# Kernel optimization log

Measured on AMD Instinct MI355X. Metric: run time of the kernel, lower is better.

Reference implementation:

```python
import jax, jax.numpy as jnp
import numpy as np

WINDOW = 7
NUM_HEADS = 12

def _relative_position_index(ws: int) -> np.ndarray:
    coords = np.stack(np.meshgrid(np.arange(ws), np.arange(ws), indexing='ij'))  # (2, ws, ws)
    flat = coords.reshape(2, -1)  # (2, N)
    rel = flat[:, :, None] - flat[:, None, :]  # (2, N, N)
    rel = rel.transpose(1, 2, 0).copy()
    rel[:, :, 0] += ws - 1
    rel[:, :, 1] += ws - 1
    rel[:, :, 0] *= 2 * ws - 1
    return rel.sum(-1)  # (N, N) int

REL_IDX = jnp.asarray(_relative_position_index(WINDOW))  # (49, 49)

def setup_inputs() -> dict:
    key = jax.random.key(0)
    ks = jax.random.split(key, 7)
    B_, N, C = 2048, 49, 384
    nW = 64
    return {
        'x': jax.random.normal(ks[0], (B_, N, C), jnp.float32),
        'mask': jax.random.normal(ks[1], (nW, N, N), jnp.float32),
        'qkv_w': jax.random.normal(ks[2], (3 * C, C), jnp.float32) * 0.02,
        'qkv_b': jax.random.normal(ks[3], (3 * C,), jnp.float32) * 0.02,
        'proj_w': jax.random.normal(ks[4], (C, C), jnp.float32) * 0.02,
        'proj_b': jax.random.normal(ks[5], (C,), jnp.float32) * 0.02,
        'rel_bias_table': jax.random.normal(ks[6], ((2 * WINDOW - 1) ** 2, NUM_HEADS), jnp.float32) * 0.02,
    }

def reference(x, mask, qkv_w, qkv_b, proj_w, proj_b, rel_bias_table):
    B_, N, C = x.shape
    H = NUM_HEADS
    D = C // H
    scale = D ** -0.5
    # fused qkv projection: (B_, N, 3C) -> (3, B_, H, N, D)
    qkv = (x @ qkv_w.T + qkv_b).reshape(B_, N, 3, H, D).transpose(2, 0, 3, 1, 4)
    q, k, v = qkv[0], qkv[1], qkv[2]
    attn = jnp.einsum('bhnd,bhmd->bhnm', q, k) * scale  # (B_, H, N, N)
    # relative position bias gather: (N, N, H) -> (H, N, N)
    bias = rel_bias_table[REL_IDX].transpose(2, 0, 1)
    attn = attn + bias[None]
    nW = mask.shape[0]
    B = B_ // nW
    attn = attn.reshape(B, nW, H, N, N) + mask[None, :, None]
    attn = attn.reshape(B_, H, N, N)
    attn = jax.nn.softmax(attn, axis=-1)
    out = jnp.einsum('bhnm,bhmd->bnhd', attn, v).reshape(B_, N, C)
    return out @ proj_w.T + proj_b
```

## Files before the change

kernel.cpp:

```cpp
#include <hip/hip_runtime.h>
#include <hip/hip_bf16.h>
#include <stdint.h>
#include <stddef.h>

typedef __attribute__((ext_vector_type(8))) short short8;
typedef __attribute__((ext_vector_type(4))) float floatx4;

#define GLDS16(gptr, lptr)                                                         \
  __builtin_amdgcn_global_load_lds(                                                \
      (const __attribute__((address_space(1))) void*)(gptr),                       \
      (__attribute__((address_space(3))) void*)(lptr), 16, 0, 0)

#define MTOT  100352
#define KDIM  384
#define NQKV  1152
#define NPROJ 384

static __device__ __forceinline__ unsigned short bfu(float f) {
    __hip_bfloat16 h = __float2bfloat16(f);
    return *(unsigned short*)&h;
}

__global__ void cvt_kernel(const float* __restrict__ in,
                           __hip_bfloat16* __restrict__ out, int n4) {
    int i = blockIdx.x * blockDim.x + threadIdx.x;
    if (i >= n4) return;
    float4 v = ((const float4*)in)[i];
    __hip_bfloat16* o = out + (size_t)i * 4;
    o[0] = __float2bfloat16(v.x);
    o[1] = __float2bfloat16(v.y);
    o[2] = __float2bfloat16(v.z);
    o[3] = __float2bfloat16(v.w);
}

__global__ void build_bias_kernel(const float* __restrict__ tbl,
                                  const float* __restrict__ mask,
                                  float* __restrict__ comb) {
    int tid = blockIdx.x * 256 + threadIdx.x;
    if (tid >= 12 * 64 * 49 * 52) return;
    int hw = tid / 2548;
    int nm = tid - hw * 2548;
    int row = nm / 52;
    int col = nm - row * 52;
    int h = hw >> 6;
    int w2 = hw & 63;
    float v = -1e30f;
    if (col < 49) {
        int i1 = row / 7, j1 = row - i1 * 7;
        int i2 = col / 7, j2 = col - i2 * 7;
        int ridx = (i1 - i2 + 6) * 13 + (j1 - j2 + 6);
        v = tbl[ridx * 12 + h] + mask[(size_t)w2 * 2401 + row * 49 + col];
    }
    comb[tid] = v;
}

template <int EPI>
__global__ __launch_bounds__(256, 4) void gemm_bt_kernel(
    const __hip_bfloat16* __restrict__ A, const __hip_bfloat16* __restrict__ B,
    const float* __restrict__ bias, float* __restrict__ Cout,
    __hip_bfloat16* __restrict__ qbuf, __hip_bfloat16* __restrict__ kbuf,
    __hip_bfloat16* __restrict__ vbuf, int N, int NBN, int vt_mode) {
    __shared__ __hip_bfloat16 sA[128 * 64];
    __shared__ __hip_bfloat16 sB[128 * 64];
    const int t = threadIdx.x;
    const int per_chunk = 16 * NBN;
    const int chunk = blockIdx.x / per_chunk;
    const int rr = blockIdx.x - chunk * per_chunk;
    const int bn = rr >> 4;
    const int bm = chunk * 16 + (rr & 15);

    const int lane = t & 63;
    const int w = t >> 6;
    const int wm = w & 1, wn = w >> 1;
    const int quad = lane >> 4, l15 = lane & 15;
    const int srow = t >> 3;
    const int scg = t & 7;
    const int sg = scg ^ (srow & 7);
    const int rsw = l15 & 7;

    const __hip_bfloat16* Ab = A + (size_t)bm * 128 * KDIM;
    const __hip_bfloat16* Bb = B + (size_t)bn * 128 * KDIM;

    const floatx4 fzero = {0.f, 0.f, 0.f, 0.f};
    floatx4 acc[4][4];
#pragma unroll
    for (int i = 0; i < 4; ++i)
#pragma unroll
        for (int j = 0; j < 4; ++j) acc[i][j] = fzero;

    for (int kk = 0; kk < KDIM; kk += 64) {
#pragma unroll
        for (int i = 0; i < 4; ++i) {
            const int r0 = srow + i * 32;
            GLDS16(Ab + (size_t)r0 * KDIM + kk + sg * 8, &sA[r0 * 64 + scg * 8]);
            GLDS16(Bb + (size_t)r0 * KDIM + kk + sg * 8, &sB[r0 * 64 + scg * 8]);
        }
        __syncthreads();
#pragma unroll
        for (int kk2 = 0; kk2 < 2; ++kk2) {
            short8 af[4], bf[4];
#pragma unroll
            for (int i = 0; i < 4; ++i)
                af[i] = *(const short8*)&sA[(wm * 64 + i * 16 + l15) * 64 +
                                            ((kk2 * 4 + quad) ^ rsw) * 8];
#pragma unroll
            for (int j = 0; j < 4; ++j)
                bf[j] = *(const short8*)&sB[(wn * 64 + j * 16 + l15) * 64 +
                                            ((kk2 * 4 + quad) ^ rsw) * 8];
#pragma unroll
            for (int i = 0; i < 4; ++i)
#pragma unroll
                for (int j = 0; j < 4; ++j)
                    acc[i][j] = __builtin_amdgcn_mfma_f32_16x16x32_bf16(
                        af[i], bf[j], acc[i][j], 0, 0, 0);
        }
        __syncthreads();
    }

    int colv[4];
    float bv4[4];
#pragma unroll
    for (int j = 0; j < 4; ++j) {
        colv[j] = bn * 128 + wn * 64 + j * 16 + l15;
        bv4[j] = bias[colv[j]];
    }

    if (EPI == 0) {
        const float scale = 0.17677669529663687f;
        int partv[4], hv4[4], dv4[4];
#pragma unroll
        for (int j = 0; j < 4; ++j) {
            partv[j] = colv[j] >= 768 ? 2 : (colv[j] >= 384 ? 1 : 0);
            int within = colv[j] - partv[j] * 384;
            hv4[j] = within >> 5;
            dv4[j] = within & 31;
        }
#pragma unroll
        for (int i = 0; i < 4; ++i) {
#pragma unroll
            for (int r = 0; r < 4; ++r) {
                const int row = bm * 128 + wm * 64 + i * 16 + quad * 4 + r;
                const int b = row / 49;
                const int nn = row - b * 49;
#pragma unroll
                for (int j = 0; j < 4; ++j) {
                    const float val = acc[i][j][r] + bv4[j];
                    const size_t bh = (size_t)b * 12 + hv4[j];
                    if (partv[j] == 0)
                        qbuf[(bh * 49 + nn) * 32 + dv4[j]] =
                            __float2bfloat16(val * scale);
                    else if (partv[j] == 1)
                        kbuf[(bh * 49 + nn) * 32 + dv4[j]] = __float2bfloat16(val);
                    else {
                        if (vt_mode)
                            vbuf[(bh * 32 + dv4[j]) * 56 + nn] = __float2bfloat16(val);
                        else
                            vbuf[(bh * 49 + nn) * 32 + dv4[j]] = __float2bfloat16(val);
                    }
                }
            }
        }
    } else {
#pragma unroll
        for (int i = 0; i < 4; ++i) {
#pragma unroll
            for (int r = 0; r < 4; ++r) {
                const int row = bm * 128 + wm * 64 + i * 16 + quad * 4 + r;
#pragma unroll
                for (int j = 0; j < 4; ++j)
                    Cout[(size_t)row * N + colv[j]] = acc[i][j][r] + bv4[j];
            }
        }
    }
}

template <int VT>
__global__ __launch_bounds__(64) void attn_kernel(
    const __hip_bfloat16* __restrict__ qbuf,
    const __hip_bfloat16* __restrict__ kbuf,
    const __hip_bfloat16* __restrict__ vslab,
    const float* __restrict__ comb,
    __hip_bfloat16* __restrict__ attn_out) {
    __shared__ unsigned short sP[64 * 72];
    const int id = blockIdx.x;
    const int h = id >> 11;
    const int rem = id & 2047;
    const int w = rem >> 5;
    const int b = rem & 31;
    const int b_ = b * 64 + w;
    const int lane = threadIdx.x;
    const int quad = lane >> 4, l15 = lane & 15;
    const size_t bh = (size_t)b_ * 12 + h;
    const short* qb = (const short*)qbuf + bh * 1568;
    const short* kb = (const short*)kbuf + bh * 1568;
    const short* vb = (const short*)vslab + bh * (VT ? 1792 : 1568);

    const floatx4 fzero = {0.f, 0.f, 0.f, 0.f};

    short8 bQ[4], aK[4];
#pragma unroll
    for (int im = 0; im < 4; ++im) {
        int m = im * 16 + l15;
        m = m > 48 ? 48 : m;
        bQ[im] = *(const short8*)(qb + m * 32 + quad * 8);
    }
#pragma unroll
    for (int jn = 0; jn < 4; ++jn) {
        int n = jn * 16 + l15;
        n = n > 48 ? 48 : n;
        aK[jn] = *(const short8*)(kb + n * 32 + quad * 8);
    }

    floatx4 ST[4][4];
#pragma unroll
    for (int im = 0; im < 4; ++im)
#pragma unroll
        for (int jn = 0; jn < 4; ++jn)
            ST[im][jn] = __builtin_amdgcn_mfma_f32_16x16x32_bf16(aK[jn], bQ[im],
                                                                 fzero, 0, 0, 0);

    const float* cb = comb + (size_t)(h * 64 + w) * 2548;
#pragma unroll
    for (int im = 0; im < 4; ++im) {
        const int m = im * 16 + l15;
        const int mrow = m > 48 ? 48 : m;
        const float* rp = cb + mrow * 52;
        float v[16];
#pragma unroll
        for (int jn = 0; jn < 3; ++jn) {
            float4 c4 = *(const float4*)(rp + jn * 16 + quad * 4);
            v[jn * 4 + 0] = ST[im][jn][0] + c4.x;
            v[jn * 4 + 1] = ST[im][jn][1] + c4.y;
            v[jn * 4 + 2] = ST[im][jn][2] + c4.z;
            v[jn * 4 + 3] = ST[im][jn][3] + c4.w;
        }
        {
            const float s48 = rp[48];
            v[12] = (quad == 0) ? (ST[im][3][0] + s48) : -1e30f;
            v[13] = -1e30f;
            v[14] = -1e30f;
            v[15] = -1e30f;
        }
        float mx = v[0];
#pragma unroll
        for (int q = 1; q < 16; ++q) mx = fmaxf(mx, v[q]);
        mx = fmaxf(mx, __shfl_xor(mx, 16));
        mx = fmaxf(mx, __shfl_xor(mx, 32));
        float sum = 0.f;
#pragma unroll
        for (int q = 0; q < 16; ++q) {
            v[q] = __expf(v[q] - mx);
            sum += v[q];
        }
        sum += __shfl_xor(sum, 16);
        sum += __shfl_xor(sum, 32);
        const float inv = 1.0f / sum;
#pragma unroll
        for (int jn = 0; jn < 4; ++jn) {
            uint2 pk;
            pk.x = (unsigned int)bfu(v[jn * 4 + 0] * inv) |
                   ((unsigned int)bfu(v[jn * 4 + 1] * inv) << 16);
            pk.y = (unsigned int)bfu(v[jn * 4 + 2] * inv) |
                   ((unsigned int)bfu(v[jn * 4 + 3] * inv) << 16);
            *(uint2*)&sP[m * 72 + jn * 16 + quad * 4] = pk;
        }
    }
    __syncthreads();

    short8 aP[4][2];
#pragma unroll
    for (int im = 0; im < 4; ++im)
#pragma unroll
        for (int kk = 0; kk < 2; ++kk)
            aP[im][kk] =
                *(const short8*)&sP[(im * 16 + l15) * 72 + kk * 32 + quad * 8];

    short8 bV[2][2];
    if (VT) {
#pragma unroll
        for (int jd = 0; jd < 2; ++jd)
#pragma unroll
            for (int kk = 0; kk < 2; ++kk) {
                int n0 = kk * 32 + quad * 8;
                n0 = n0 > 48 ? 48 : n0;
                bV[jd][kk] = *(const short8*)(vb + (jd * 16 + l15) * 56 + n0);
            }
    } else {
#pragma unroll
        for (int jd = 0; jd < 2; ++jd)
#pragma unroll
            for (int kk = 0; kk < 2; ++kk) {
                short8 tmp;
#pragma unroll
                for (int jj = 0; jj < 8; ++jj) {
                    int k = kk * 32 + quad * 8 + jj;
                    k = k > 48 ? 48 : k;
                    tmp[jj] = vb[k * 32 + jd * 16 + l15];
                }
                bV[jd][kk] = tmp;
            }
    }

    floatx4 O[4][2];
#pragma unroll
    for (int im = 0; im < 4; ++im)
#pragma unroll
        for (int jd = 0; jd < 2; ++jd) {
            floatx4 o = __builtin_amdgcn_mfma_f32_16x16x32_bf16(aP[im][0], bV[jd][0],
                                                                fzero, 0, 0, 0);
            o = __builtin_amdgcn_mfma_f32_16x16x32_bf16(aP[im][1], bV[jd][1], o, 0,
                                                        0, 0);
            O[im][jd] = o;
        }

#pragma unroll
    for (int im = 0; im < 4; ++im) {
#pragma unroll
        for (int r = 0; r < 4; ++r) {
            const int m = im * 16 + quad * 4 + r;
            if (m < 49) {
#pragma unroll
                for (int jd = 0; jd < 2; ++jd)
                    attn_out[((size_t)b_ * 49 + m) * 384 + h * 32 + jd * 16 + l15] =
                        __float2bfloat16(O[im][jd][r]);
            }
        }
    }
}

extern "C" void kernel_launch(void* const* d_in, const int* in_sizes, int n_in,
                              void* d_out, int out_size, void* d_ws,
                              size_t ws_size, hipStream_t stream) {
    (void)in_sizes; (void)n_in; (void)out_size;
    const float* x      = (const float*)d_in[0];
    const float* mask   = (const float*)d_in[1];
    const float* qkv_w  = (const float*)d_in[2];
    const float* qkv_b  = (const float*)d_in[3];
    const float* proj_w = (const float*)d_in[4];
    const float* proj_b = (const float*)d_in[5];
    const float* tbl    = (const float*)d_in[6];
    float* out = (float*)d_out;
    char* ws = (char*)d_ws;

    __hip_bfloat16* x_bf  = (__hip_bfloat16*)(ws);
    __hip_bfloat16* wq_bf = (__hip_bfloat16*)(ws + 77070336);
    float*          comb  = (float*)(ws + 77070336);
    __hip_bfloat16* wp_bf = (__hip_bfloat16*)(ws + 84897792);
    __hip_bfloat16* q_buf = (__hip_bfloat16*)(ws + 85192704);
    __hip_bfloat16* k_buf = (__hip_bfloat16*)(ws + 162263040);
    __hip_bfloat16* v_slab = (__hip_bfloat16*)(ws + 239333376);
    __hip_bfloat16* attn_out = x_bf;

    const int vt = (ws_size >= (size_t)327413760) ? 1 : 0;

    cvt_kernel<<<(MTOT * KDIM / 4 + 255) / 256, 256, 0, stream>>>(x, x_bf,
                                                                  MTOT * KDIM / 4);
    cvt_kernel<<<(NQKV * KDIM / 4 + 255) / 256, 256, 0, stream>>>(
        qkv_w, wq_bf, NQKV * KDIM / 4);
    cvt_kernel<<<(NPROJ * KDIM / 4 + 255) / 256, 256, 0, stream>>>(
        proj_w, wp_bf, NPROJ * KDIM / 4);
    gemm_bt_kernel<0><<<784 * 9, 256, 0, stream>>>(x_bf, wq_bf, qkv_b, nullptr,
                                                   q_buf, k_buf, v_slab, NQKV, 9,
                                                   vt);
    build_bias_kernel<<<(12 * 64 * 49 * 52 + 255) / 256, 256, 0, stream>>>(
        tbl, mask, comb);
    if (vt)
        attn_kernel<1><<<2048 * 12, 64, 0, stream>>>(q_buf, k_buf, v_slab, comb,
                                                     attn_out);
    else
        attn_kernel<0><<<2048 * 12, 64, 0, stream>>>(q_buf, k_buf, v_slab, comb,
                                                     attn_out);
    gemm_bt_kernel<1><<<784 * 3, 256, 0, stream>>>(attn_out, wp_bf, proj_b, out,
                                                   nullptr, nullptr, nullptr,
                                                   NPROJ, 3, 0);
}
```

Measured before the change: 612.5 us.

## Store QKV as row-major bf16 with vectorized epilogues and stage V via LDS

The QKV GEMM now writes a plain row-major bf16 [M,1152] buffer. Swapping the MFMA operands lets each lane hold four consecutive columns, so the epilogue packs them into 8-byte stores instead of scattered 2-byte writes into per-head Q/K/V layouts. The projection GEMM epilogue likewise uses float4 stores. The attention kernel reads Q/K/V with strided row loads, stages V through shared memory to transpose it, and writes its output as packed 8-byte stores. This trades strided reads in attention, which touch many rows at a 2304-byte stride, for coalesced GEMM epilogue writes and drops the transposed-V workspace path.

Result: faster. 557.8 us (-8.9%).

```diff
diff --git a/kernel.cpp b/kernel.cpp
--- a/kernel.cpp
+++ b/kernel.cpp
@@ -16,9 +16,9 @@
 #define NQKV  1152
 #define NPROJ 384
 
-static __device__ __forceinline__ unsigned short bfu(float f) {
+static __device__ __forceinline__ unsigned int bfu(float f) {
     __hip_bfloat16 h = __float2bfloat16(f);
-    return *(unsigned short*)&h;
+    return (unsigned int)*(unsigned short*)&h;
 }
 
 __global__ void cvt_kernel(const float* __restrict__ in,
@@ -58,8 +58,7 @@
 __global__ __launch_bounds__(256, 4) void gemm_bt_kernel(
     const __hip_bfloat16* __restrict__ A, const __hip_bfloat16* __restrict__ B,
     const float* __restrict__ bias, float* __restrict__ Cout,
-    __hip_bfloat16* __restrict__ qbuf, __hip_bfloat16* __restrict__ kbuf,
-    __hip_bfloat16* __restrict__ vbuf, int N, int NBN, int vt_mode) {
+    __hip_bfloat16* __restrict__ Cbf, int N, int NBN) {
     __shared__ __hip_bfloat16 sA[128 * 64];
     __shared__ __hip_bfloat16 sB[128 * 64];
     const int t = threadIdx.x;
@@ -112,76 +111,54 @@
 #pragma unroll
                 for (int j = 0; j < 4; ++j)
                     acc[i][j] = __builtin_amdgcn_mfma_f32_16x16x32_bf16(
-                        af[i], bf[j], acc[i][j], 0, 0, 0);
+                        bf[j], af[i], acc[i][j], 0, 0, 0);
         }
         __syncthreads();
-    }
-
-    int colv[4];
-    float bv4[4];
-#pragma unroll
-    for (int j = 0; j < 4; ++j) {
-        colv[j] = bn * 128 + wn * 64 + j * 16 + l15;
-        bv4[j] = bias[colv[j]];
     }
 
     if (EPI == 0) {
         const float scale = 0.17677669529663687f;
-        int partv[4], hv4[4], dv4[4];
-#pragma unroll
-        for (int j = 0; j < 4; ++j) {
-            partv[j] = colv[j] >= 768 ? 2 : (colv[j] >= 384 ? 1 : 0);
-            int within = colv[j] - partv[j] * 384;
-            hv4[j] = within >> 5;
-            dv4[j] = within & 31;
-        }
 #pragma unroll
         for (int i = 0; i < 4; ++i) {
-#pragma unroll
-            for (int r = 0; r < 4; ++r) {
-                const int row = bm * 128 + wm * 64 + i * 16 + quad * 4 + r;
-                const int b = row / 49;
-                const int nn = row - b * 49;
-#pragma unroll
-                for (int j = 0; j < 4; ++j) {
-                    const float val = acc[i][j][r] + bv4[j];
-                    const size_t bh = (size_t)b * 12 + hv4[j];
-                    if (partv[j] == 0)
-                        qbuf[(bh * 49 + nn) * 32 + dv4[j]] =
-                            __float2bfloat16(val * scale);
-                    else if (partv[j] == 1)
-                        kbuf[(bh * 49 + nn) * 32 + dv4[j]] = __float2bfloat16(val);
-                    else {
-                        if (vt_mode)
-                            vbuf[(bh * 32 + dv4[j]) * 56 + nn] = __float2bfloat16(val);
-                        else
-                            vbuf[(bh * 49 + nn) * 32 + dv4[j]] = __float2bfloat16(val);
-                    }
-                }
+            const int m = bm * 128 + wm * 64 + i * 16 + l15;
+#pragma unroll
+            for (int j = 0; j < 4; ++j) {
+                const int f0 = bn * 128 + wn * 64 + j * 16 + quad * 4;
+                const float4 bv = *(const float4*)&bias[f0];
+                const float sc = (f0 < 384) ? scale : 1.0f;
+                uint2 pk;
+                pk.x = bfu((acc[i][j][0] + bv.x) * sc) |
+                       (bfu((acc[i][j][1] + bv.y) * sc) << 16);
+                pk.y = bfu((acc[i][j][2] + bv.z) * sc) |
+                       (bfu((acc[i][j][3] + bv.w) * sc) << 16);
+                *(uint2*)&Cbf[(size_t)m * NQKV + f0] = pk;
             }
         }
     } else {
 #pragma unroll
         for (int i = 0; i < 4; ++i) {
-#pragma unroll
-            for (int r = 0; r < 4; ++r) {
-                const int row = bm * 128 + wm * 64 + i * 16 + quad * 4 + r;
-#pragma unroll
-                for (int j = 0; j < 4; ++j)
-                    Cout[(size_t)row * N + colv[j]] = acc[i][j][r] + bv4[j];
+            const int m = bm * 128 + wm * 64 + i * 16 + l15;
+#pragma unroll
+            for (int j = 0; j < 4; ++j) {
+                const int f0 = bn * 128 + wn * 64 + j * 16 + quad * 4;
+                const float4 bv = *(const float4*)&bias[f0];
+                float4 o;
+                o.x = acc[i][j][0] + bv.x;
+                o.y = acc[i][j][1] + bv.y;
+                o.z = acc[i][j][2] + bv.z;
+                o.w = acc[i][j][3] + bv.w;
+                *(float4*)&Cout[(size_t)m * N + f0] = o;
             }
         }
     }
 }
 
-template <int VT>
 __global__ __launch_bounds__(64) void attn_kernel(
-    const __hip_bfloat16* __restrict__ qbuf,
-    const __hip_bfloat16* __restrict__ kbuf,
-    const __hip_bfloat16* __restrict__ vslab,
+    const __hip_bfloat16* __restrict__ qkv,
     const float* __restrict__ comb,
     __hip_bfloat16* __restrict__ attn_out) {
     __shared__ unsigned short sP[64 * 72];
+    __shared__ unsigned short sVB[4][66][8];
     const int id = blockIdx.x;
     const int h = id >> 11;
     const int rem = id & 2047;
@@ -190,10 +167,7 @@
     const int b_ = b * 64 + w;
     const int lane = threadIdx.x;
     const int quad = lane >> 4, l15 = lane & 15;
-    const size_t bh = (size_t)b_ * 12 + h;
-    const short* qb = (const short*)qbuf + bh * 1568;
-    const short* kb = (const short*)kbuf + bh * 1568;
-    const short* vb = (const short*)vslab + bh * (VT ? 1792 : 1568);
+    const short* base = (const short*)qkv + (size_t)b_ * 49 * 1152 + h * 32;
 
     const floatx4 fzero = {0.f, 0.f, 0.f, 0.f};
 
@@ -202,13 +176,22 @@
     for (int im = 0; im < 4; ++im) {
         int m = im * 16 + l15;
         m = m > 48 ? 48 : m;
-        bQ[im] = *(const short8*)(qb + m * 32 + quad * 8);
+        bQ[im] = *(const short8*)(base + (size_t)m * 1152 + quad * 8);
     }
 #pragma unroll
     for (int jn = 0; jn < 4; ++jn) {
         int n = jn * 16 + l15;
         n = n > 48 ? 48 : n;
-        aK[jn] = *(const short8*)(kb + n * 32 + quad * 8);
+        aK[jn] = *(const short8*)(base + (size_t)n * 1152 + 384 + quad * 8);
+    }
+    const short8 zero8 = {0, 0, 0, 0, 0, 0, 0, 0};
+#pragma unroll
+    for (int jn = 0; jn < 4; ++jn) {
+        const int n = jn * 16 + l15;
+        const int nc = n > 48 ? 48 : n;
+        short8 vv = *(const short8*)(base + (size_t)nc * 1152 + 768 + quad * 8);
+        if (n > 48) vv = zero8;
+        *(short8*)&sVB[quad][n][0] = vv;
     }
 
     floatx4 ST[4][4];
@@ -258,10 +241,8 @@
 #pragma unroll
         for (int jn = 0; jn < 4; ++jn) {
             uint2 pk;
-            pk.x = (unsigned int)bfu(v[jn * 4 + 0] * inv) |
-                   ((unsigned int)bfu(v[jn * 4 + 1] * inv) << 16);
-            pk.y = (unsigned int)bfu(v[jn * 4 + 2] * inv) |
-                   ((unsigned int)bfu(v[jn * 4 + 3] * inv) << 16);
+            pk.x = bfu(v[jn * 4 + 0] * inv) | (bfu(v[jn * 4 + 1] * inv) << 16);
+            pk.y = bfu(v[jn * 4 + 2] * inv) | (bfu(v[jn * 4 + 3] * inv) << 16);
             *(uint2*)&sP[m * 72 + jn * 16 + quad * 4] = pk;
         }
     }
@@ -276,29 +257,18 @@
                 *(const short8*)&sP[(im * 16 + l15) * 72 + kk * 32 + quad * 8];
 
     short8 bV[2][2];
-    if (VT) {
-#pragma unroll
-        for (int jd = 0; jd < 2; ++jd)
-#pragma unroll
-            for (int kk = 0; kk < 2; ++kk) {
-                int n0 = kk * 32 + quad * 8;
-                n0 = n0 > 48 ? 48 : n0;
-                bV[jd][kk] = *(const short8*)(vb + (jd * 16 + l15) * 56 + n0);
-            }
-    } else {
-#pragma unroll
-        for (int jd = 0; jd < 2; ++jd)
-#pragma unroll
-            for (int kk = 0; kk < 2; ++kk) {
-                short8 tmp;
-#pragma unroll
-                for (int jj = 0; jj < 8; ++jj) {
-                    int k = kk * 32 + quad * 8 + jj;
-                    k = k > 48 ? 48 : k;
-                    tmp[jj] = vb[k * 32 + jd * 16 + l15];
-                }
-                bV[jd][kk] = tmp;
-            }
+#pragma unroll
+    for (int jd = 0; jd < 2; ++jd) {
+        const int d = jd * 16 + l15;
+        const int db = d >> 3, dl = d & 7;
+#pragma unroll
+        for (int kk = 0; kk < 2; ++kk) {
+            short8 tmp;
+#pragma unroll
+            for (int jj = 0; jj < 8; ++jj)
+                tmp[jj] = (short)sVB[db][kk * 32 + quad * 8 + jj][dl];
+            bV[jd][kk] = tmp;
+        }
     }
 
     floatx4 O[4][2];
@@ -306,23 +276,25 @@
     for (int im = 0; im < 4; ++im)
 #pragma unroll
         for (int jd = 0; jd < 2; ++jd) {
-            floatx4 o = __builtin_amdgcn_mfma_f32_16x16x32_bf16(aP[im][0], bV[jd][0],
-                                                                fzero, 0, 0, 0);
-            o = __builtin_amdgcn_mfma_f32_16x16x32_bf16(aP[im][1], bV[jd][1], o, 0,
+            floatx4 o = __builtin_amdgcn_mfma_f32_16x16x32_bf16(bV[jd][0],
+                                                                aP[im][0], fzero,
+                                                                0, 0, 0);
+            o = __builtin_amdgcn_mfma_f32_16x16x32_bf16(bV[jd][1], aP[im][1], o, 0,
                                                         0, 0);
             O[im][jd] = o;
         }
 
 #pragma unroll
     for (int im = 0; im < 4; ++im) {
-#pragma unroll
-        for (int r = 0; r < 4; ++r) {
-            const int m = im * 16 + quad * 4 + r;
-            if (m < 49) {
-#pragma unroll
-                for (int jd = 0; jd < 2; ++jd)
-                    attn_out[((size_t)b_ * 49 + m) * 384 + h * 32 + jd * 16 + l15] =
-                        __float2bfloat16(O[im][jd][r]);
+        const int m = im * 16 + l15;
+        if (m < 49) {
+#pragma unroll
+            for (int jd = 0; jd < 2; ++jd) {
+                uint2 pk;
+                pk.x = bfu(O[im][jd][0]) | (bfu(O[im][jd][1]) << 16);
+                pk.y = bfu(O[im][jd][2]) | (bfu(O[im][jd][3]) << 16);
+                *(uint2*)&attn_out[((size_t)b_ * 49 + m) * 384 + h * 32 +
+                                   jd * 16 + quad * 4] = pk;
             }
         }
     }
@@ -331,7 +303,7 @@
 extern "C" void kernel_launch(void* const* d_in, const int* in_sizes, int n_in,
                               void* d_out, int out_size, void* d_ws,
                               size_t ws_size, hipStream_t stream) {
-    (void)in_sizes; (void)n_in; (void)out_size;
+    (void)in_sizes; (void)n_in; (void)out_size; (void)ws_size;
     const float* x      = (const float*)d_in[0];
     const float* mask   = (const float*)d_in[1];
     const float* qkv_w  = (const float*)d_in[2];
@@ -342,16 +314,12 @@
     float* out = (float*)d_out;
     char* ws = (char*)d_ws;
 
-    __hip_bfloat16* x_bf  = (__hip_bfloat16*)(ws);
-    __hip_bfloat16* wq_bf = (__hip_bfloat16*)(ws + 77070336);
-    float*          comb  = (float*)(ws + 77070336);
-    __hip_bfloat16* wp_bf = (__hip_bfloat16*)(ws + 84897792);
-    __hip_bfloat16* q_buf = (__hip_bfloat16*)(ws + 85192704);
-    __hip_bfloat16* k_buf = (__hip_bfloat16*)(ws + 162263040);
-    __hip_bfloat16* v_slab = (__hip_bfloat16*)(ws + 239333376);
-    __hip_bfloat16* attn_out = x_bf;
-
-    const int vt = (ws_size >= (size_t)327413760) ? 1 : 0;
+    __hip_bfloat16* x_bf   = (__hip_bfloat16*)(ws);
+    __hip_bfloat16* wq_bf  = (__hip_bfloat16*)(ws + 77070336);
+    float*          comb   = (float*)(ws + 77070336);
+    __hip_bfloat16* wp_bf  = (__hip_bfloat16*)(ws + 84897792);
+    __hip_bfloat16* qkv_o  = (__hip_bfloat16*)(ws + 85192704);
+    __hip_bfloat16* attn_o = x_bf;
 
     cvt_kernel<<<(MTOT * KDIM / 4 + 255) / 256, 256, 0, stream>>>(x, x_bf,
                                                                   MTOT * KDIM / 4);
@@ -360,17 +328,10 @@
     cvt_kernel<<<(NPROJ * KDIM / 4 + 255) / 256, 256, 0, stream>>>(
         proj_w, wp_bf, NPROJ * KDIM / 4);
     gemm_bt_kernel<0><<<784 * 9, 256, 0, stream>>>(x_bf, wq_bf, qkv_b, nullptr,
-                                                   q_buf, k_buf, v_slab, NQKV, 9,
-                                                   vt);
+                                                   qkv_o, NQKV, 9);
     build_bias_kernel<<<(12 * 64 * 49 * 52 + 255) / 256, 256, 0, stream>>>(
         tbl, mask, comb);
-    if (vt)
-        attn_kernel<1><<<2048 * 12, 64, 0, stream>>>(q_buf, k_buf, v_slab, comb,
-                                                     attn_out);
-    else
-        attn_kernel<0><<<2048 * 12, 64, 0, stream>>>(q_buf, k_buf, v_slab, comb,
-                                                     attn_out);
-    gemm_bt_kernel<1><<<784 * 3, 256, 0, stream>>>(attn_out, wp_bf, proj_b, out,
-                                                   nullptr, nullptr, nullptr,
-                                                   NPROJ, 3, 0);
-}
+    attn_kernel<<<2048 * 12, 64, 0, stream>>>(qkv_o, comb, attn_o);
+    gemm_bt_kernel<1><<<784 * 3, 256, 0, stream>>>(attn_o, wp_bf, proj_b, out,
+                                                   nullptr, NPROJ, 3);
+}
```
